# Kernel tuning notes

Measured on AMD Instinct MI355X. Metric: run time of the kernel, lower is better.

Reference implementation:

```python
import jax, jax.numpy as jnp
import numpy as np
from jax import lax

B, T, H, W, C = 2, 16, 64, 64, 64
KT, K = 3, 3


def kernel_to_freq_3d(kernel, T, H, W):
    # kernel: (C, k_t, k_h, k_w) -> (C, T, H, W) complex freq response
    Cc, k_t, k_h, k_w = kernel.shape
    t_idx = (jnp.arange(k_t) - k_t // 2) % T
    h_idx = (jnp.arange(k_h) - k_h // 2) % H
    w_idx = (jnp.arange(k_w) - k_w // 2) % W
    tt, th, tw = jnp.meshgrid(t_idx, h_idx, w_idx, indexing='ij')
    padded = jnp.zeros((Cc, T, H, W), dtype=kernel.dtype).at[:, tt, th, tw].set(kernel)
    return jnp.fft.fftn(padded, axes=(1, 2, 3))


def mamba_op(left, right):
    a1, b1 = left
    a2, b2 = right
    return (a1 * a2, a2 * b1 + b2)


def setup_inputs() -> dict:
    key = jax.random.key(0)
    ks = jax.random.split(key, 8)
    fan_in = KT * K * K
    x = jax.random.normal(ks[0], (B, T, H, W, C), dtype=jnp.float32)
    A_kernel = jax.random.normal(ks[1], (C, KT, K, K), dtype=jnp.float32) / np.sqrt(fan_in)
    B_kernel = jax.random.normal(ks[2], (C, KT, K, K), dtype=jnp.float32) / np.sqrt(fan_in)
    forget_bias = jnp.full((C,), 2.0, dtype=jnp.float32)
    forget_scale = jnp.full((C,), 0.01, dtype=jnp.float32)
    input_bias = jnp.zeros((C,), dtype=jnp.float32)
    input_scale = jnp.full((C,), 0.01, dtype=jnp.float32)
    delta_W = jax.random.normal(ks[3], (C, C), dtype=jnp.float32) / np.sqrt(C)
    delta_b = jnp.zeros((C,), dtype=jnp.float32)
    return {"x": x, "A_kernel": A_kernel, "B_kernel": B_kernel,
            "forget_bias": forget_bias, "forget_scale": forget_scale,
            "input_bias": input_bias, "input_scale": input_scale,
            "delta_W": delta_W, "delta_b": delta_b}


def reference(x, A_kernel, B_kernel, forget_bias, forget_scale,
              input_bias, input_scale, delta_W, delta_b):
    Bb, Tt, Hh, Ww, Cc = x.shape
    # freq-domain kernels: (C,T,H,W) -> (T,1,H,W,C) for broadcasting over batch
    A_f = kernel_to_freq_3d(A_kernel, Tt, Hh, Ww).transpose(1, 2, 3, 0)[:, None]
    B_f = kernel_to_freq_3d(B_kernel, Tt, Hh, Ww).transpose(1, 2, 3, 0)[:, None]
    # input-dependent gates (real, elementwise per channel)
    forget_gate = jax.nn.sigmoid(forget_bias + forget_scale * x)
    input_gate = jax.nn.sigmoid(input_bias + input_scale * x)
    delta = jax.nn.softplus(jnp.einsum('bthwc,cd->bthwd', x, delta_W) + delta_b)
    x_f = jnp.fft.fftn(x, axes=(1, 2, 3))  # complex (B,T,H,W,C)
    # move time axis to front for the scan: (T,B,H,W,C)
    a_seq = forget_gate.transpose(1, 0, 2, 3, 4) * A_f
    b_seq = (input_gate.transpose(1, 0, 2, 3, 4)
             * delta.transpose(1, 0, 2, 3, 4)
             * B_f * x_f.transpose(1, 0, 2, 3, 4))
    _, h_all_f = lax.associative_scan(mamba_op, (a_seq, b_seq), axis=0)
    h_f = h_all_f.transpose(1, 0, 2, 3, 4)
    h = jnp.fft.ifftn(h_f, axes=(1, 2, 3)).real
    return h.astype(x.dtype)
```

## Files before the change

### kernel.cpp

```cpp
#include <hip/hip_runtime.h>
#include <math.h>

#define Bb 2
#define Tt 16
#define Hh 64
#define Ww 64
#define Cc 64
#define ST_ (Hh*Ww*Cc)
#define SB_ (Tt*Hh*Ww*Cc)

#define TWO_PI 6.2831853071795864769f

typedef __attribute__((ext_vector_type(8))) short bf16x8;
typedef __attribute__((ext_vector_type(4))) float f32x4;

#define BUF_A    0u
#define BUF_B    8388608u
#define OFF_PRE  16777216u
#define OFF_TWF  16779264u
#define OFF_THF  16783360u
#define OFF_THI  16791552u
#define OFF_TWI  16799744u

__device__ __forceinline__ float2 cmul(float2 a, float2 b) {
    return make_float2(fmaf(a.x, b.x, -a.y * b.y), fmaf(a.x, b.y, a.y * b.x));
}
__device__ __forceinline__ float2 cadd(float2 a, float2 b) { return make_float2(a.x + b.x, a.y + b.y); }
__device__ __forceinline__ float2 csub(float2 a, float2 b) { return make_float2(a.x - b.x, a.y - b.y); }

__device__ __forceinline__ unsigned bfpack(float2 f) {
    unsigned r = __float_as_uint(f.x);
    unsigned i = __float_as_uint(f.y);
    r = (r + 0x7fffu + ((r >> 16) & 1u)) >> 16;
    i = (i + 0x7fffu + ((i >> 16) & 1u)) >> 16;
    return r | (i << 16);
}
__device__ __forceinline__ float2 bfunpack(unsigned u) {
    return make_float2(__uint_as_float(u << 16), __uint_as_float(u & 0xffff0000u));
}

template <int S>
__device__ __forceinline__ void fft4(float2& a, float2& b, float2& c, float2& d) {
    float2 t0 = cadd(a, c), t1 = csub(a, c);
    float2 t2 = cadd(b, d), t3 = csub(b, d);
    a = cadd(t0, t2);
    c = csub(t0, t2);
    b = make_float2(t1.x - (float)S * t3.y, t1.y + (float)S * t3.x);
    d = make_float2(t1.x + (float)S * t3.y, t1.y - (float)S * t3.x);
}

template <int S>
__device__ __forceinline__ void fft16(float2 v[16]) {
    const float CS[10] = {1.f, 0.92387953f, 0.70710678f, 0.38268343f, 0.f,
                          -0.38268343f, -0.70710678f, -0.92387953f, -1.f, -0.92387953f};
    const float SN[10] = {0.f, 0.38268343f, 0.70710678f, 0.92387953f, 1.f,
                          0.92387953f, 0.70710678f, 0.38268343f, 0.f, -0.38268343f};
    float2 A[4][4];
#pragma unroll
    for (int j = 0; j < 4; ++j) {
        A[j][0] = v[j]; A[j][1] = v[4 + j]; A[j][2] = v[8 + j]; A[j][3] = v[12 + j];
        fft4<S>(A[j][0], A[j][1], A[j][2], A[j][3]);
#pragma unroll
        for (int k0 = 0; k0 < 4; ++k0) {
            int m = j * k0;
            float2 tw = make_float2(CS[m], (float)S * SN[m]);
            A[j][k0] = cmul(A[j][k0], tw);
        }
    }
#pragma unroll
    for (int k0 = 0; k0 < 4; ++k0) {
        fft4<S>(A[0][k0], A[1][k0], A[2][k0], A[3][k0]);
        v[k0] = A[0][k0]; v[k0 + 4] = A[1][k0]; v[k0 + 8] = A[2][k0]; v[k0 + 12] = A[3][k0];
    }
}

__global__ __launch_bounds__(256) void k_setup(const float* __restrict__ dW,
                                               unsigned* __restrict__ ws) {
    int j = blockIdx.x * 256 + threadIdx.x;
    if (j < 2048) {
        int p2 = j & 3, lane = (j >> 2) & 63, ka = (j >> 8) & 1, nt = j >> 9;
        int kb = ka * 32 + (lane >> 4) * 8 + 2 * p2;
        int ccol = (lane & 15) + 16 * nt;
        ws[OFF_PRE + j] = bfpack(make_float2(dW[kb * 64 + ccol], dW[(kb + 1) * 64 + ccol]));
        return;
    }
    int idx, table;
    if (j < 6144)       { idx = j - 2048;  table = 0; }
    else if (j < 14336) { idx = j - 6144;  table = 1; }
    else if (j < 22528) { idx = j - 14336; table = 2; }
    else                { idx = j - 22528; table = 3; }
    int p = idx & 3;
    int lane = (idx >> 2) & 63;
    int m = lane & 15, q = lane >> 4;
    int ka, r, reim;
    if (table == 0)      { ka = (idx >> 8) & 1; r = (idx >> 9) & 3;  reim = (idx >> 11) & 1; }
    else if (table == 3) { ka = (idx >> 8) & 3; r = (idx >> 10) & 3; reim = 0; }
    else                 { ka = (idx >> 8) & 3; r = (idx >> 10) & 3; reim = (idx >> 12) & 1; }
    int wp = r * 16 + m;
    int k0 = ka * 32 + q * 8 + 2 * p;
    float val[2];
#pragma unroll
    for (int dk = 0; dk < 2; ++dk) {
        int k = k0 + dk;
        float v;
        if (table == 0) {
            int a = (wp * k) & 63;
            float sn, cs; sincosf(TWO_PI * (float)a * (1.0f / 64.0f), &sn, &cs);
            v = (reim == 0) ? cs : -sn;
        } else {
            int h = k >> 1;
            int a = (wp * h) & 63;
            float sn, cs; sincosf(TWO_PI * (float)a * (1.0f / 64.0f), &sn, &cs);
            bool even = (k & 1) == 0;
            if (table == 1) {
                v = (reim == 0) ? (even ? cs : sn) : (even ? -sn : cs);
            } else if (table == 2) {
                v = (reim == 0) ? (even ? cs : -sn) : (even ? sn : cs);
                v *= (1.0f / 64.0f);
            } else {
                v = (even ? cs : -sn) * (1.0f / 64.0f);
            }
        }
        val[dk] = v;
    }
    unsigned base = (table == 0) ? OFF_TWF : (table == 1) ? OFF_THF
                  : (table == 2) ? OFF_THI : OFF_TWI;
    ws[base + idx] = bfpack(make_float2(val[0], val[1]));
}

__global__ __launch_bounds__(256) void k_dft_w_fwd(const float* __restrict__ x,
                                                   unsigned* __restrict__ X1,
                                                   const uint4* __restrict__ T) {
    __shared__ unsigned zw[64 * 66];
    int tid = threadIdx.x;
    int s = blockIdx.x;
    const float* src = x + (size_t)s * 4096;
    for (int idx = tid; idx < 2048; idx += 256) {
        int i = idx >> 6, c = idx & 63;
        zw[c * 66 + i] = bfpack(make_float2(src[i * 128 + c], src[i * 128 + 64 + c]));
    }
    __syncthreads();

    int r = tid >> 6, lane = tid & 63;
    int m = lane & 15, q = lane >> 4;
    union U48 { uint4 u4; uint2 u2[2]; unsigned u[4]; bf16x8 v8; };
    U48 Are[2], Aim[2], Bf;
#pragma unroll
    for (int ka = 0; ka < 2; ++ka) {
        Are[ka].u4 = T[((0 * 4 + r) * 2 + ka) * 64 + lane];
        Aim[ka].u4 = T[((1 * 4 + r) * 2 + ka) * 64 + lane];
    }
    f32x4 ar[4], ai[4];
#pragma unroll
    for (int nt = 0; nt < 4; ++nt) { ar[nt] = (f32x4){0.f,0.f,0.f,0.f}; ai[nt] = (f32x4){0.f,0.f,0.f,0.f}; }
#pragma unroll
    for (int nt = 0; nt < 4; ++nt) {
        int cc = m + 16 * nt;
#pragma unroll
        for (int ka = 0; ka < 2; ++ka) {
            int i0 = ka * 16 + q * 4;
            Bf.u2[0] = *(const uint2*)&zw[cc * 66 + i0];
            Bf.u2[1] = *(const uint2*)&zw[cc * 66 + i0 + 2];
            ar[nt] = __builtin_amdgcn_mfma_f32_16x16x32_bf16(Are[ka].v8, Bf.v8, ar[nt], 0, 0, 0);
            ai[nt] = __builtin_amdgcn_mfma_f32_16x16x32_bf16(Aim[ka].v8, Bf.v8, ai[nt], 0, 0, 0);
        }
    }
    int bt = s >> 6, h = s & 63;
    size_t ob = (size_t)bt * 262144 + (size_t)h * 64;
#pragma unroll
    for (int nt = 0; nt < 4; ++nt) {
        int cc = m + 16 * nt;
#pragma unroll
        for (int reg = 0; reg < 4; ++reg) {
            int wp = r * 16 + q * 4 + reg;
            X1[ob + (size_t)wp * 4096 + cc] = bfpack(make_float2(ar[nt][reg], ai[nt][reg]));
        }
    }
}

__global__ __launch_bounds__(256) void k_dft_h_fwd(const unsigned* __restrict__ X1,
                                                   unsigned* __restrict__ X2,
                                                   const uint4* __restrict__ T) {
    __shared__ unsigned zs[64 * 66];
    int tid = threadIdx.x;
    int s = blockIdx.x;
    const unsigned* src = X1 + (size_t)s * 4096;
    for (int i = tid; i < 4096; i += 256) {
        int h = i >> 6, c = i & 63;
        zs[c * 66 + h] = src[i];
    }
    __syncthreads();

    int r = tid >> 6, lane = tid & 63;
    int m = lane & 15, q = lane >> 4;
    union U48 { uint4 u4; uint2 u2[2]; unsigned u[4]; bf16x8 v8; };
    U48 Are[4], Aim[4], Bf;
#pragma unroll
    for (int ka = 0; ka < 4; ++ka) {
        Are[ka].u4 = T[((0 * 4 + r) * 4 + ka) * 64 + lane];
        Aim[ka].u4 = T[((1 * 4 + r) * 4 + ka) * 64 + lane];
    }
    f32x4 ar[4], ai[4];
#pragma unroll
    for (int nt = 0; nt < 4; ++nt) { ar[nt] = (f32x4){0.f,0.f,0.f,0.f}; ai[nt] = (f32x4){0.f,0.f,0.f,0.f}; }
#pragma unroll
    for (int nt = 0; nt < 4; ++nt) {
        int cc = m + 16 * nt;
#pragma unroll
        for (int ka = 0; ka < 4; ++ka) {
            int h0 = ka * 16 + q * 4;
            Bf.u2[0] = *(const uint2*)&zs[cc * 66 + h0];
            Bf.u2[1] = *(const uint2*)&zs[cc * 66 + h0 + 2];
            ar[nt] = __builtin_amdgcn_mfma_f32_16x16x32_bf16(Are[ka].v8, Bf.v8, ar[nt], 0, 0, 0);
            ai[nt] = __builtin_amdgcn_mfma_f32_16x16x32_bf16(Aim[ka].v8, Bf.v8, ai[nt], 0, 0, 0);
        }
    }
    int b = s >> 10, t = (s >> 6) & 15, w = s & 63;
    size_t ob = (size_t)b * 4194304 + (size_t)w * 1024 + (size_t)t * 64;
#pragma unroll
    for (int nt = 0; nt < 4; ++nt) {
        int cc = m + 16 * nt;
#pragma unroll
        for (int reg = 0; reg < 4; ++reg) {
            int hp = r * 16 + q * 4 + reg;
            X2[ob + (size_t)hp * 65536 + cc] = bfpack(make_float2(ar[nt][reg], ai[nt][reg]));
        }
    }
}

__global__ __launch_bounds__(256) void k_dft_h_inv(const unsigned* __restrict__ X3,
                                                   unsigned* __restrict__ X4,
                                                   const uint4* __restrict__ T) {
    __shared__ unsigned zs[64 * 66];
    int tid = threadIdx.x;
    int s = blockIdx.x;
    const unsigned* src = X3 + (size_t)s * 4096;
    for (int i = tid; i < 4096; i += 256) {
        int h = i >> 6, c = i & 63;
        zs[c * 66 + h] = src[i];
    }
    __syncthreads();

    int r = tid >> 6, lane = tid & 63;
    int m = lane & 15, q = lane >> 4;
    union U48 { uint4 u4; uint2 u2[2]; unsigned u[4]; bf16x8 v8; };
    U48 Are[4], Aim[4], Bf;
#pragma unroll
    for (int ka = 0; ka < 4; ++ka) {
        Are[ka].u4 = T[((0 * 4 + r) * 4 + ka) * 64 + lane];
        Aim[ka].u4 = T[((1 * 4 + r) * 4 + ka) * 64 + lane];
    }
    f32x4 ar[4], ai[4];
#pragma unroll
    for (int nt = 0; nt < 4; ++nt) { ar[nt] = (f32x4){0.f,0.f,0.f,0.f}; ai[nt] = (f32x4){0.f,0.f,0.f,0.f}; }
#pragma unroll
    for (int nt = 0; nt < 4; ++nt) {
        int cc = m + 16 * nt;
#pragma unroll
        for (int ka = 0; ka < 4; ++ka) {
            int h0 = ka * 16 + q * 4;
            Bf.u2[0] = *(const uint2*)&zs[cc * 66 + h0];
            Bf.u2[1] = *(const uint2*)&zs[cc * 66 + h0 + 2];
            ar[nt] = __builtin_amdgcn_mfma_f32_16x16x32_bf16(Are[ka].v8, Bf.v8, ar[nt], 0, 0, 0);
            ai[nt] = __builtin_amdgcn_mfma_f32_16x16x32_bf16(Aim[ka].v8, Bf.v8, ai[nt], 0, 0, 0);
        }
    }
    int bt = s >> 6, w = s & 63;
    size_t ob = (size_t)bt * 262144 + (size_t)w * 64;
#pragma unroll
    for (int nt = 0; nt < 4; ++nt) {
        int cc = m + 16 * nt;
#pragma unroll
        for (int reg = 0; reg < 4; ++reg) {
            int hp = r * 16 + q * 4 + reg;
            X4[ob + (size_t)hp * 4096 + cc] = bfpack(make_float2(ar[nt][reg], ai[nt][reg]));
        }
    }
}

__global__ __launch_bounds__(256) void k_dft_w_inv(const unsigned* __restrict__ X4,
                                                   float* __restrict__ out,
                                                   const uint4* __restrict__ T) {
    __shared__ unsigned zs[64 * 66];
    int tid = threadIdx.x;
    int s = blockIdx.x;
    const unsigned* src = X4 + (size_t)s * 4096;
    for (int i = tid; i < 4096; i += 256) {
        int w = i >> 6, c = i & 63;
        zs[c * 66 + w] = src[i];
    }
    __syncthreads();

    int r = tid >> 6, lane = tid & 63;
    int m = lane & 15, q = lane >> 4;
    union U48 { uint4 u4; uint2 u2[2]; unsigned u[4]; bf16x8 v8; };
    U48 Are[4], Bf;
#pragma unroll
    for (int ka = 0; ka < 4; ++ka)
        Are[ka].u4 = T[(r * 4 + ka) * 64 + lane];
    f32x4 ar[4];
#pragma unroll
    for (int nt = 0; nt < 4; ++nt) ar[nt] = (f32x4){0.f,0.f,0.f,0.f};
#pragma unroll
    for (int nt = 0; nt < 4; ++nt) {
        int cc = m + 16 * nt;
#pragma unroll
        for (int ka = 0; ka < 4; ++ka) {
            int w0 = ka * 16 + q * 4;
            Bf.u2[0] = *(const uint2*)&zs[cc * 66 + w0];
            Bf.u2[1] = *(const uint2*)&zs[cc * 66 + w0 + 2];
            ar[nt] = __builtin_amdgcn_mfma_f32_16x16x32_bf16(Are[ka].v8, Bf.v8, ar[nt], 0, 0, 0);
        }
    }
    float* dst = out + (size_t)s * 4096;
#pragma unroll
    for (int nt = 0; nt < 4; ++nt) {
        int cc = m + 16 * nt;
#pragma unroll
        for (int reg = 0; reg < 4; ++reg) {
            int wp = r * 16 + q * 4 + reg;
            dst[wp * 64 + cc] = ar[nt][reg];
        }
    }
}

__global__ __launch_bounds__(256) void k_mid(
    const float* __restrict__ x, const unsigned* __restrict__ X2,
    unsigned* __restrict__ X3,
    const float* __restrict__ Ak, const float* __restrict__ Bk,
    const float* __restrict__ fb, const float* __restrict__ fs,
    const float* __restrict__ ib, const float* __restrict__ isc_,
    const uint4* __restrict__ pre, const float* __restrict__ db) {
    const float CT[16] = {1.f, 0.9238795f, 0.7071068f, 0.3826834f, 0.f, -0.3826834f,
                          -0.7071068f, -0.9238795f, -1.f, -0.9238795f, -0.7071068f,
                          -0.3826834f, 0.f, 0.3826834f, 0.7071068f, 0.9238795f};
    const float SN[16] = {0.f, 0.3826834f, 0.7071068f, 0.9238795f, 1.f, 0.9238795f,
                          0.7071068f, 0.3826834f, 0.f, -0.3826834f, -0.7071068f,
                          -0.9238795f, -1.f, -0.9238795f, -0.7071068f, -0.3826834f};
    __shared__ float Akl[1728], Bkl[1728];
    __shared__ __align__(16) float xs[4][16 * 68 + 4];

    int tid = threadIdx.x;
    int g = tid >> 6, lane = tid & 63;
    int c = lane;
    int site = blockIdx.x * 4 + g;
    int b = site >> 12, hw = site & 4095;
    int h = hw >> 6, w = hw & 63;
    size_t base = (size_t)b * SB_ + (size_t)hw * 64;

    for (int i = tid; i < 1728; i += 256) { Akl[i] = Ak[i]; Bkl[i] = Bk[i]; }

    float xv[16];
    float2 v[16];
    const unsigned* src2 = X2 + (size_t)site * 1024;
#pragma unroll
    for (int t = 0; t < 16; ++t) {
        xv[t] = x[base + (size_t)t * ST_ + c];
        v[t] = bfunpack(src2[t * 64 + c]);
    }
#pragma unroll
    for (int t = 0; t < 16; ++t) xs[g][t * 68 + c] = xv[t];
    __syncthreads();

    int m = lane & 15, q = lane >> 4;
    bf16x8 Afrag[2];
#pragma unroll
    for (int ka = 0; ka < 2; ++ka) {
        int d0 = ka * 32 + q * 8;
        const float* p = &xs[g][m * 68 + d0];
        float4 f0 = *(const float4*)p;
        float4 f1 = *(const float4*)(p + 4);
        union { bf16x8 v8; unsigned u[4]; } U;
        U.u[0] = bfpack(make_float2(f0.x, f0.y));
        U.u[1] = bfpack(make_float2(f0.z, f0.w));
        U.u[2] = bfpack(make_float2(f1.x, f1.y));
        U.u[3] = bfpack(make_float2(f1.z, f1.w));
        Afrag[ka] = U.v8;
    }
#pragma unroll
    for (int nt = 0; nt < 4; ++nt) {
        int ccol = m + 16 * nt;
        float dbn = db[ccol];
        f32x4 acc = {dbn, dbn, dbn, dbn};
#pragma unroll
        for (int ka = 0; ka < 2; ++ka) {
            union { bf16x8 v8; uint4 u4; } Ub;
            Ub.u4 = pre[(nt * 2 + ka) * 64 + lane];
            acc = __builtin_amdgcn_mfma_f32_16x16x32_bf16(Afrag[ka], Ub.v8, acc, 0, 0, 0);
        }
#pragma unroll
        for (int reg = 0; reg < 4; ++reg)
            xs[g][(q * 4 + reg) * 68 + ccol] = acc[reg];
    }

    float sh, ch; sincosf(TWO_PI * (float)h / 64.0f, &sh, &ch);
    float sw, cw; sincosf(TWO_PI * (float)w / 64.0f, &sw, &cw);
    float2 eh[3] = { make_float2(ch, sh), make_float2(1.f, 0.f), make_float2(ch, -sh) };
    float2 ew[3] = { make_float2(cw, sw), make_float2(1.f, 0.f), make_float2(cw, -sw) };
    float2 GA[3], GB[3];
#pragma unroll
    for (int kt = 0; kt < 3; ++kt) { GA[kt] = make_float2(0.f, 0.f); GB[kt] = make_float2(0.f, 0.f); }
#pragma unroll
    for (int kh = 0; kh < 3; ++kh) {
#pragma unroll
        for (int kw = 0; kw < 3; ++kw) {
            float2 e = cmul(eh[kh], ew[kw]);
#pragma unroll
            for (int kt = 0; kt < 3; ++kt) {
                float ka = Akl[c * 27 + kt * 9 + kh * 3 + kw];
                float kb = Bkl[c * 27 + kt * 9 + kh * 3 + kw];
                GA[kt].x = fmaf(ka, e.x, GA[kt].x);
                GA[kt].y = fmaf(ka, e.y, GA[kt].y);
                GB[kt].x = fmaf(kb, e.x, GB[kt].x);
                GB[kt].y = fmaf(kb, e.y, GB[kt].y);
            }
        }
    }
    float fbc = fb[c], fsc = fs[c], ibc = ib[c], iscv = isc_[c];

    fft16<-1>(v);
    __syncthreads();

    float delta_raw[16];
#pragma unroll
    for (int t = 0; t < 16; ++t) delta_raw[t] = xs[g][t * 68 + c];

    float2 hv = make_float2(0.f, 0.f);
#pragma unroll
    for (int t = 0; t < 16; ++t) {
        float ct = CT[t], st = SN[t];
        float2 Af, Bf;
        Af.x = GA[1].x + ct * (GA[0].x + GA[2].x) - st * (GA[0].y - GA[2].y);
        Af.y = GA[1].y + ct * (GA[0].y + GA[2].y) + st * (GA[0].x - GA[2].x);
        Bf.x = GB[1].x + ct * (GB[0].x + GB[2].x) - st * (GB[0].y - GB[2].y);
        Bf.y = GB[1].y + ct * (GB[0].y + GB[2].y) + st * (GB[0].x - GB[2].x);

        float xc = xv[t];
        float fg  = __builtin_amdgcn_rcpf(1.f + __expf(-(fbc + fsc * xc)));
        float igv = __builtin_amdgcn_rcpf(1.f + __expf(-(ibc + iscv * xc)));
        float dot = delta_raw[t];
        float delta = (dot > 20.f) ? dot : __logf(1.f + __expf(dot));

        float sR = igv * delta;
        float2 bbv;
        bbv.x = sR * (Bf.x * v[t].x - Bf.y * v[t].y);
        bbv.y = sR * (Bf.x * v[t].y + Bf.y * v[t].x);
        float2 av = make_float2(fg * Af.x, fg * Af.y);
        float2 nh;
        nh.x = av.x * hv.x - av.y * hv.y + bbv.x;
        nh.y = av.x * hv.y + av.y * hv.x + bbv.y;
        hv = nh;
        v[t] = hv;
    }

    fft16<1>(v);

    size_t ob = (size_t)b * 4194304 + (size_t)w * 4096 + (size_t)h * 64 + c;
#pragma unroll
    for (int t = 0; t < 16; ++t) {
        float2 o = make_float2(v[t].x * 0.0625f, v[t].y * 0.0625f);
        X3[ob + (size_t)t * 262144] = bfpack(o);
    }
}

extern "C" void kernel_launch(void* const* d_in, const int* in_sizes, int n_in,
                              void* d_out, int out_size, void* d_ws, size_t ws_size,
                              hipStream_t stream) {
    const float* x   = (const float*)d_in[0];
    const float* Ak  = (const float*)d_in[1];
    const float* Bk  = (const float*)d_in[2];
    const float* fb  = (const float*)d_in[3];
    const float* fs  = (const float*)d_in[4];
    const float* ib  = (const float*)d_in[5];
    const float* is_ = (const float*)d_in[6];
    const float* dW  = (const float*)d_in[7];
    const float* db  = (const float*)d_in[8];
    float* out = (float*)d_out;
    unsigned* ws = (unsigned*)d_ws;
    unsigned* A = ws + BUF_A;
    unsigned* B = ws + BUF_B;

    k_setup<<<104, 256, 0, stream>>>(dW, ws);
    k_dft_w_fwd<<<Bb * Tt * Hh, 256, 0, stream>>>(x, A, (const uint4*)(ws + OFF_TWF));
    k_dft_h_fwd<<<Bb * Tt * Ww, 256, 0, stream>>>(A, B, (const uint4*)(ws + OFF_THF));
    k_mid<<<(Bb * Hh * Ww) / 4, 256, 0, stream>>>(x, B, A, Ak, Bk, fb, fs, ib, is_,
                                                  (const uint4*)(ws + OFF_PRE), db);
    k_dft_h_inv<<<Bb * Tt * Ww, 256, 0, stream>>>(A, B, (const uint4*)(ws + OFF_THI));
    k_dft_w_inv<<<Bb * Tt * Hh, 256, 0, stream>>>(B, out, (const uint4*)(ws + OFF_TWI));
}
```

Measured before the change: 171.7 us.

## Fold setup into forward W-DFT, vectorize global loads, stage coalesced stores via LDS

```diff
diff --git a/kernel.cpp b/kernel.cpp
--- a/kernel.cpp
+++ b/kernel.cpp
@@ -17,10 +17,9 @@
 #define BUF_A    0u
 #define BUF_B    8388608u
 #define OFF_PRE  16777216u
-#define OFF_TWF  16779264u
-#define OFF_THF  16783360u
-#define OFF_THI  16791552u
-#define OFF_TWI  16799744u
+#define OFF_THF  16779264u
+#define OFF_THI  16787456u
+#define OFF_TWI  16795648u
 
 __device__ __forceinline__ float2 cmul(float2 a, float2 b) {
     return make_float2(fmaf(a.x, b.x, -a.y * b.y), fmaf(a.x, b.y, a.y * b.x));
@@ -74,81 +73,92 @@
     }
 }
 
-__global__ __launch_bounds__(256) void k_setup(const float* __restrict__ dW,
-                                               unsigned* __restrict__ ws) {
-    int j = blockIdx.x * 256 + threadIdx.x;
-    if (j < 2048) {
-        int p2 = j & 3, lane = (j >> 2) & 63, ka = (j >> 8) & 1, nt = j >> 9;
-        int kb = ka * 32 + (lane >> 4) * 8 + 2 * p2;
-        int ccol = (lane & 15) + 16 * nt;
-        ws[OFF_PRE + j] = bfpack(make_float2(dW[kb * 64 + ccol], dW[(kb + 1) * 64 + ccol]));
-        return;
-    }
-    int idx, table;
-    if (j < 6144)       { idx = j - 2048;  table = 0; }
-    else if (j < 14336) { idx = j - 6144;  table = 1; }
-    else if (j < 22528) { idx = j - 14336; table = 2; }
-    else                { idx = j - 22528; table = 3; }
-    int p = idx & 3;
-    int lane = (idx >> 2) & 63;
-    int m = lane & 15, q = lane >> 4;
-    int ka, r, reim;
-    if (table == 0)      { ka = (idx >> 8) & 1; r = (idx >> 9) & 3;  reim = (idx >> 11) & 1; }
-    else if (table == 3) { ka = (idx >> 8) & 3; r = (idx >> 10) & 3; reim = 0; }
-    else                 { ka = (idx >> 8) & 3; r = (idx >> 10) & 3; reim = (idx >> 12) & 1; }
-    int wp = r * 16 + m;
-    int k0 = ka * 32 + q * 8 + 2 * p;
-    float val[2];
-#pragma unroll
-    for (int dk = 0; dk < 2; ++dk) {
-        int k = k0 + dk;
-        float v;
-        if (table == 0) {
-            int a = (wp * k) & 63;
-            float sn, cs; sincosf(TWO_PI * (float)a * (1.0f / 64.0f), &sn, &cs);
-            v = (reim == 0) ? cs : -sn;
-        } else {
-            int h = k >> 1;
-            int a = (wp * h) & 63;
-            float sn, cs; sincosf(TWO_PI * (float)a * (1.0f / 64.0f), &sn, &cs);
-            bool even = (k & 1) == 0;
-            if (table == 1) {
-                v = (reim == 0) ? (even ? cs : sn) : (even ? -sn : cs);
-            } else if (table == 2) {
-                v = (reim == 0) ? (even ? cs : -sn) : (even ? sn : cs);
-                v *= (1.0f / 64.0f);
-            } else {
-                v = (even ? cs : -sn) * (1.0f / 64.0f);
-            }
-        }
-        val[dk] = v;
-    }
-    unsigned base = (table == 0) ? OFF_TWF : (table == 1) ? OFF_THF
-                  : (table == 2) ? OFF_THI : OFF_TWI;
-    ws[base + idx] = bfpack(make_float2(val[0], val[1]));
-}
-
 __global__ __launch_bounds__(256) void k_dft_w_fwd(const float* __restrict__ x,
                                                    unsigned* __restrict__ X1,
-                                                   const uint4* __restrict__ T) {
-    __shared__ unsigned zw[64 * 66];
+                                                   const float* __restrict__ dW,
+                                                   unsigned* __restrict__ ws) {
+    __shared__ unsigned zs[64 * 68];
     int tid = threadIdx.x;
+
+    if (blockIdx.x == 0) {
+        for (int j = tid; j < 22528; j += 256) {
+            if (j < 2048) {
+                int p2 = j & 3, lane = (j >> 2) & 63, ka = (j >> 8) & 1, nt = j >> 9;
+                int kb = ka * 32 + (lane >> 4) * 8 + 2 * p2;
+                int ccol = (lane & 15) + 16 * nt;
+                ws[OFF_PRE + j] = bfpack(make_float2(dW[kb * 64 + ccol], dW[(kb + 1) * 64 + ccol]));
+            } else {
+                int idx, table;
+                if (j < 10240)      { idx = j - 2048;  table = 1; }
+                else if (j < 18432) { idx = j - 10240; table = 2; }
+                else                { idx = j - 18432; table = 3; }
+                int p = idx & 3;
+                int lane = (idx >> 2) & 63;
+                int m = lane & 15, q = lane >> 4;
+                int ka, r, reim;
+                if (table == 3) { ka = (idx >> 8) & 3; r = (idx >> 10) & 3; reim = 0; }
+                else            { ka = (idx >> 8) & 3; r = (idx >> 10) & 3; reim = (idx >> 12) & 1; }
+                int wp = r * 16 + m;
+                int k0 = ka * 32 + q * 8 + 2 * p;
+                float val[2];
+#pragma unroll
+                for (int dk = 0; dk < 2; ++dk) {
+                    int k = k0 + dk;
+                    int h = k >> 1;
+                    int a = (wp * h) & 63;
+                    float sn, cs; sincosf(TWO_PI * (float)a * (1.0f / 64.0f), &sn, &cs);
+                    bool even = (k & 1) == 0;
+                    float v;
+                    if (table == 1) {
+                        v = (reim == 0) ? (even ? cs : sn) : (even ? -sn : cs);
+                    } else if (table == 2) {
+                        v = ((reim == 0) ? (even ? cs : -sn) : (even ? sn : cs)) * (1.0f / 64.0f);
+                    } else {
+                        v = (even ? cs : -sn) * (1.0f / 64.0f);
+                    }
+                    val[dk] = v;
+                }
+                unsigned base = (table == 1) ? OFF_THF : (table == 2) ? OFF_THI : OFF_TWI;
+                ws[base + idx] = bfpack(make_float2(val[0], val[1]));
+            }
+        }
+    }
+
     int s = blockIdx.x;
-    const float* src = x + (size_t)s * 4096;
-    for (int idx = tid; idx < 2048; idx += 256) {
-        int i = idx >> 6, c = idx & 63;
-        zw[c * 66 + i] = bfpack(make_float2(src[i * 128 + c], src[i * 128 + 64 + c]));
+    const float4* src4 = (const float4*)(x + (size_t)s * 4096);
+#pragma unroll
+    for (int k = 0; k < 2; ++k) {
+        int idx = tid + k * 256;
+        int i = idx >> 4, cc4 = idx & 15, c0 = cc4 * 4;
+        float4 A = src4[(2 * i) * 16 + cc4];
+        float4 B = src4[(2 * i + 1) * 16 + cc4];
+        zs[(c0 + 0) * 66 + i] = bfpack(make_float2(A.x, B.x));
+        zs[(c0 + 1) * 66 + i] = bfpack(make_float2(A.y, B.y));
+        zs[(c0 + 2) * 66 + i] = bfpack(make_float2(A.z, B.z));
+        zs[(c0 + 3) * 66 + i] = bfpack(make_float2(A.w, B.w));
     }
     __syncthreads();
 
     int r = tid >> 6, lane = tid & 63;
     int m = lane & 15, q = lane >> 4;
+    int wp0 = r * 16 + m;
     union U48 { uint4 u4; uint2 u2[2]; unsigned u[4]; bf16x8 v8; };
     U48 Are[2], Aim[2], Bf;
 #pragma unroll
     for (int ka = 0; ka < 2; ++ka) {
-        Are[ka].u4 = T[((0 * 4 + r) * 2 + ka) * 64 + lane];
-        Aim[ka].u4 = T[((1 * 4 + r) * 2 + ka) * 64 + lane];
+#pragma unroll
+        for (int p = 0; p < 4; ++p) {
+            float re[2], im[2];
+#pragma unroll
+            for (int dk = 0; dk < 2; ++dk) {
+                int k = ka * 32 + q * 8 + 2 * p + dk;
+                int a = (wp0 * k) & 63;
+                float sn, cs; sincosf(TWO_PI * (float)a * (1.0f / 64.0f), &sn, &cs);
+                re[dk] = cs; im[dk] = -sn;
+            }
+            Are[ka].u[p] = bfpack(make_float2(re[0], re[1]));
+            Aim[ka].u[p] = bfpack(make_float2(im[0], im[1]));
+        }
     }
     f32x4 ar[4], ai[4];
 #pragma unroll
@@ -159,35 +169,47 @@
 #pragma unroll
         for (int ka = 0; ka < 2; ++ka) {
             int i0 = ka * 16 + q * 4;
-            Bf.u2[0] = *(const uint2*)&zw[cc * 66 + i0];
-            Bf.u2[1] = *(const uint2*)&zw[cc * 66 + i0 + 2];
+            Bf.u2[0] = *(const uint2*)&zs[cc * 66 + i0];
+            Bf.u2[1] = *(const uint2*)&zs[cc * 66 + i0 + 2];
             ar[nt] = __builtin_amdgcn_mfma_f32_16x16x32_bf16(Are[ka].v8, Bf.v8, ar[nt], 0, 0, 0);
             ai[nt] = __builtin_amdgcn_mfma_f32_16x16x32_bf16(Aim[ka].v8, Bf.v8, ai[nt], 0, 0, 0);
         }
     }
+    __syncthreads();
+#pragma unroll
+    for (int nt = 0; nt < 4; ++nt) {
+        int cc = m + 16 * nt;
+#pragma unroll
+        for (int reg = 0; reg < 4; ++reg)
+            zs[(r * 16 + q * 4 + reg) * 68 + cc] = bfpack(make_float2(ar[nt][reg], ai[nt][reg]));
+    }
+    __syncthreads();
     int bt = s >> 6, h = s & 63;
-    size_t ob = (size_t)bt * 262144 + (size_t)h * 64;
-#pragma unroll
-    for (int nt = 0; nt < 4; ++nt) {
-        int cc = m + 16 * nt;
-#pragma unroll
-        for (int reg = 0; reg < 4; ++reg) {
-            int wp = r * 16 + q * 4 + reg;
-            X1[ob + (size_t)wp * 4096 + cc] = bfpack(make_float2(ar[nt][reg], ai[nt][reg]));
-        }
-    }
-}
-
-__global__ __launch_bounds__(256) void k_dft_h_fwd(const unsigned* __restrict__ X1,
-                                                   unsigned* __restrict__ X2,
-                                                   const uint4* __restrict__ T) {
-    __shared__ unsigned zs[64 * 66];
-    int tid = threadIdx.x;
-    int s = blockIdx.x;
-    const unsigned* src = X1 + (size_t)s * 4096;
-    for (int i = tid; i < 4096; i += 256) {
-        int h = i >> 6, c = i & 63;
-        zs[c * 66 + h] = src[i];
+    unsigned* dst = X1 + (size_t)bt * 262144 + (size_t)h * 64;
+#pragma unroll
+    for (int rr = 0; rr < 4; ++rr) {
+        int g = tid + 256 * rr;
+        int row = g >> 4, c0 = (g & 15) * 4;
+        *(uint4*)&dst[(size_t)row * 4096 + c0] = *(const uint4*)&zs[row * 68 + c0];
+    }
+}
+
+template <int OSTRIDE>
+__device__ __forceinline__ void dft_h_body(const unsigned* __restrict__ src,
+                                           unsigned* __restrict__ dst,
+                                           const uint4* __restrict__ T,
+                                           unsigned* zs, int tid) {
+    const uint4* src4 = (const uint4*)src;
+#pragma unroll
+    for (int k = 0; k < 4; ++k) {
+        int idx4 = tid + k * 256;
+        uint4 d = src4[idx4];
+        int i = idx4 * 4;
+        int h = i >> 6, c0 = i & 63;
+        zs[(c0 + 0) * 66 + h] = d.x;
+        zs[(c0 + 1) * 66 + h] = d.y;
+        zs[(c0 + 2) * 66 + h] = d.z;
+        zs[(c0 + 3) * 66 + h] = d.w;
     }
     __syncthreads();
 
@@ -215,79 +237,60 @@
             ai[nt] = __builtin_amdgcn_mfma_f32_16x16x32_bf16(Aim[ka].v8, Bf.v8, ai[nt], 0, 0, 0);
         }
     }
+    __syncthreads();
+#pragma unroll
+    for (int nt = 0; nt < 4; ++nt) {
+        int cc = m + 16 * nt;
+#pragma unroll
+        for (int reg = 0; reg < 4; ++reg)
+            zs[(r * 16 + q * 4 + reg) * 68 + cc] = bfpack(make_float2(ar[nt][reg], ai[nt][reg]));
+    }
+    __syncthreads();
+#pragma unroll
+    for (int rr = 0; rr < 4; ++rr) {
+        int g = tid + 256 * rr;
+        int row = g >> 4, c0 = (g & 15) * 4;
+        *(uint4*)&dst[(size_t)row * OSTRIDE + c0] = *(const uint4*)&zs[row * 68 + c0];
+    }
+}
+
+__global__ __launch_bounds__(256) void k_dft_h_fwd(const unsigned* __restrict__ X1,
+                                                   unsigned* __restrict__ X2,
+                                                   const uint4* __restrict__ T) {
+    __shared__ unsigned zs[64 * 68];
+    int s = blockIdx.x;
     int b = s >> 10, t = (s >> 6) & 15, w = s & 63;
-    size_t ob = (size_t)b * 4194304 + (size_t)w * 1024 + (size_t)t * 64;
-#pragma unroll
-    for (int nt = 0; nt < 4; ++nt) {
-        int cc = m + 16 * nt;
-#pragma unroll
-        for (int reg = 0; reg < 4; ++reg) {
-            int hp = r * 16 + q * 4 + reg;
-            X2[ob + (size_t)hp * 65536 + cc] = bfpack(make_float2(ar[nt][reg], ai[nt][reg]));
-        }
-    }
+    unsigned* dst = X2 + (size_t)b * 4194304 + (size_t)w * 1024 + (size_t)t * 64;
+    dft_h_body<65536>(X1 + (size_t)s * 4096, dst, T, zs, threadIdx.x);
 }
 
 __global__ __launch_bounds__(256) void k_dft_h_inv(const unsigned* __restrict__ X3,
                                                    unsigned* __restrict__ X4,
                                                    const uint4* __restrict__ T) {
-    __shared__ unsigned zs[64 * 66];
-    int tid = threadIdx.x;
+    __shared__ unsigned zs[64 * 68];
     int s = blockIdx.x;
-    const unsigned* src = X3 + (size_t)s * 4096;
-    for (int i = tid; i < 4096; i += 256) {
-        int h = i >> 6, c = i & 63;
-        zs[c * 66 + h] = src[i];
-    }
-    __syncthreads();
-
-    int r = tid >> 6, lane = tid & 63;
-    int m = lane & 15, q = lane >> 4;
-    union U48 { uint4 u4; uint2 u2[2]; unsigned u[4]; bf16x8 v8; };
-    U48 Are[4], Aim[4], Bf;
-#pragma unroll
-    for (int ka = 0; ka < 4; ++ka) {
-        Are[ka].u4 = T[((0 * 4 + r) * 4 + ka) * 64 + lane];
-        Aim[ka].u4 = T[((1 * 4 + r) * 4 + ka) * 64 + lane];
-    }
-    f32x4 ar[4], ai[4];
-#pragma unroll
-    for (int nt = 0; nt < 4; ++nt) { ar[nt] = (f32x4){0.f,0.f,0.f,0.f}; ai[nt] = (f32x4){0.f,0.f,0.f,0.f}; }
-#pragma unroll
-    for (int nt = 0; nt < 4; ++nt) {
-        int cc = m + 16 * nt;
-#pragma unroll
-        for (int ka = 0; ka < 4; ++ka) {
-            int h0 = ka * 16 + q * 4;
-            Bf.u2[0] = *(const uint2*)&zs[cc * 66 + h0];
-            Bf.u2[1] = *(const uint2*)&zs[cc * 66 + h0 + 2];
-            ar[nt] = __builtin_amdgcn_mfma_f32_16x16x32_bf16(Are[ka].v8, Bf.v8, ar[nt], 0, 0, 0);
-            ai[nt] = __builtin_amdgcn_mfma_f32_16x16x32_bf16(Aim[ka].v8, Bf.v8, ai[nt], 0, 0, 0);
-        }
-    }
     int bt = s >> 6, w = s & 63;
-    size_t ob = (size_t)bt * 262144 + (size_t)w * 64;
-#pragma unroll
-    for (int nt = 0; nt < 4; ++nt) {
-        int cc = m + 16 * nt;
-#pragma unroll
-        for (int reg = 0; reg < 4; ++reg) {
-            int hp = r * 16 + q * 4 + reg;
-            X4[ob + (size_t)hp * 4096 + cc] = bfpack(make_float2(ar[nt][reg], ai[nt][reg]));
-        }
-    }
+    unsigned* dst = X4 + (size_t)bt * 262144 + (size_t)w * 64;
+    dft_h_body<4096>(X3 + (size_t)s * 4096, dst, T, zs, threadIdx.x);
 }
 
 __global__ __launch_bounds__(256) void k_dft_w_inv(const unsigned* __restrict__ X4,
                                                    float* __restrict__ out,
                                                    const uint4* __restrict__ T) {
-    __shared__ unsigned zs[64 * 66];
+    __shared__ unsigned zs[64 * 68];
     int tid = threadIdx.x;
     int s = blockIdx.x;
-    const unsigned* src = X4 + (size_t)s * 4096;
-    for (int i = tid; i < 4096; i += 256) {
-        int w = i >> 6, c = i & 63;
-        zs[c * 66 + w] = src[i];
+    const uint4* src4 = (const uint4*)(X4 + (size_t)s * 4096);
+#pragma unroll
+    for (int k = 0; k < 4; ++k) {
+        int idx4 = tid + k * 256;
+        uint4 d = src4[idx4];
+        int i = idx4 * 4;
+        int w = i >> 6, c0 = i & 63;
+        zs[(c0 + 0) * 66 + w] = d.x;
+        zs[(c0 + 1) * 66 + w] = d.y;
+        zs[(c0 + 2) * 66 + w] = d.z;
+        zs[(c0 + 3) * 66 + w] = d.w;
     }
     __syncthreads();
 
@@ -312,15 +315,22 @@
             ar[nt] = __builtin_amdgcn_mfma_f32_16x16x32_bf16(Are[ka].v8, Bf.v8, ar[nt], 0, 0, 0);
         }
     }
+    __syncthreads();
+    float* fz = (float*)zs;
+#pragma unroll
+    for (int nt = 0; nt < 4; ++nt) {
+        int cc = m + 16 * nt;
+#pragma unroll
+        for (int reg = 0; reg < 4; ++reg)
+            fz[(r * 16 + q * 4 + reg) * 68 + cc] = ar[nt][reg];
+    }
+    __syncthreads();
     float* dst = out + (size_t)s * 4096;
 #pragma unroll
-    for (int nt = 0; nt < 4; ++nt) {
-        int cc = m + 16 * nt;
-#pragma unroll
-        for (int reg = 0; reg < 4; ++reg) {
-            int wp = r * 16 + q * 4 + reg;
-            dst[wp * 64 + cc] = ar[nt][reg];
-        }
+    for (int rr = 0; rr < 4; ++rr) {
+        int g = tid + 256 * rr;
+        int row = g >> 4, c0 = (g & 15) * 4;
+        *(float4*)&dst[row * 64 + c0] = *(const float4*)&fz[row * 68 + c0];
     }
 }
 
@@ -338,7 +348,7 @@
                           0.7071068f, 0.3826834f, 0.f, -0.3826834f, -0.7071068f,
                           -0.9238795f, -1.f, -0.9238795f, -0.7071068f, -0.3826834f};
     __shared__ float Akl[1728], Bkl[1728];
-    __shared__ __align__(16) float xs[4][16 * 68 + 4];
+    __shared__ __align__(16) float xs[4][16 * 68];
 
     int tid = threadIdx.x;
     int g = tid >> 6, lane = tid & 63;
@@ -348,18 +358,26 @@
     int h = hw >> 6, w = hw & 63;
     size_t base = (size_t)b * SB_ + (size_t)hw * 64;
 
-    for (int i = tid; i < 1728; i += 256) { Akl[i] = Ak[i]; Bkl[i] = Bk[i]; }
-
-    float xv[16];
+    for (int i = tid; i < 432; i += 256) {
+        *(float4*)&Akl[4 * i] = *(const float4*)&Ak[4 * i];
+        *(float4*)&Bkl[4 * i] = *(const float4*)&Bk[4 * i];
+    }
+
     float2 v[16];
     const unsigned* src2 = X2 + (size_t)site * 1024;
 #pragma unroll
-    for (int t = 0; t < 16; ++t) {
-        xv[t] = x[base + (size_t)t * ST_ + c];
-        v[t] = bfunpack(src2[t * 64 + c]);
-    }
-#pragma unroll
-    for (int t = 0; t < 16; ++t) xs[g][t * 68 + c] = xv[t];
+    for (int t = 0; t < 16; ++t) v[t] = bfunpack(src2[t * 64 + c]);
+
+#pragma unroll
+    for (int k = 0; k < 4; ++k) {
+        int idx = lane + 64 * k;
+        int t = idx >> 4, c0 = (idx & 15) * 4;
+        float4 px = *(const float4*)&x[base + (size_t)t * ST_ + c0];
+        *(float4*)&xs[g][t * 68 + c0] = px;
+    }
+    float xv[16];
+#pragma unroll
+    for (int t = 0; t < 16; ++t) xv[t] = xs[g][t * 68 + c];
     __syncthreads();
 
     int m = lane & 15, q = lane >> 4;
@@ -419,7 +437,6 @@
     float fbc = fb[c], fsc = fs[c], ibc = ib[c], iscv = isc_[c];
 
     fft16<-1>(v);
-    __syncthreads();
 
     float delta_raw[16];
 #pragma unroll
@@ -480,8 +497,7 @@
     unsigned* A = ws + BUF_A;
     unsigned* B = ws + BUF_B;
 
-    k_setup<<<104, 256, 0, stream>>>(dW, ws);
-    k_dft_w_fwd<<<Bb * Tt * Hh, 256, 0, stream>>>(x, A, (const uint4*)(ws + OFF_TWF));
+    k_dft_w_fwd<<<Bb * Tt * Hh, 256, 0, stream>>>(x, A, dW, ws);
     k_dft_h_fwd<<<Bb * Tt * Ww, 256, 0, stream>>>(A, B, (const uint4*)(ws + OFF_THF));
     k_mid<<<(Bb * Hh * Ww) / 4, 256, 0, stream>>>(x, B, A, Ak, Bk, fb, fs, ib, is_,
                                                   (const uint4*)(ws + OFF_PRE), db);
```

Result: slower. 199.0 us (+15.9%).
